# Kernel tuning notes

Measured on AMD Instinct MI355X. Metric: run time of the kernel, lower is better.

The kernel has to match this reference:

```python
import jax, jax.numpy as jnp
import numpy as np

NEG_SLOPE = 0.01  # torch F.leaky_relu default


def setup_inputs() -> dict:
    key = jax.random.key(0)
    k1, k2, k3, k4, k5 = jax.random.split(key, 5)
    N, E, IN_DIM, OUT_DIM = 100000, 1600000, 128, 64
    h = jax.random.normal(k1, (N, IN_DIM), dtype=jnp.float32)
    src = jax.random.randint(k2, (E,), 0, N, dtype=jnp.int64)
    dst = jax.random.randint(k3, (E,), 0, N, dtype=jnp.int64)
    # xavier_normal-ish scaled params
    W1 = jax.random.normal(k4, (OUT_DIM, IN_DIM), dtype=jnp.float32) * (2.0 / (IN_DIM + OUT_DIM)) ** 0.5
    Wa = jax.random.normal(k5, (1, 2 * OUT_DIM), dtype=jnp.float32) * (2.0 / (2 * OUT_DIM + 1)) ** 0.5
    return {"h": h, "src": src, "dst": dst, "W1": W1, "Wa": Wa}


def reference(h, src, dst, W1, Wa):
    N = h.shape[0]
    D = W1.shape[0]
    z = h @ W1.T  # [N, D]
    z_src = z[src]  # [E, D] gather
    z_dst = z[dst]  # [E, D] gather
    a_src, a_dst = Wa[0, :D], Wa[0, D:]
    # attn_fc(concat(z_src, z_dst)) == z_src@a_src + z_dst@a_dst
    e = z_src @ a_src + z_dst @ a_dst  # [E]
    e = jnp.where(e >= 0, e, NEG_SLOPE * e)  # leaky_relu
    # segment softmax over incoming edges of each dst node
    e_max = jax.ops.segment_max(e, dst, num_segments=N)
    e_max = jnp.where(jnp.isfinite(e_max), e_max, 0.0)  # empty segments
    e_exp = jnp.exp(e - e_max[dst])
    denom = jax.ops.segment_sum(e_exp, dst, num_segments=N)
    alpha = e_exp / jnp.maximum(denom, 1e-16)[dst]  # [E]
    # weighted scatter-sum of source messages
    h_out = jax.ops.segment_sum(alpha[:, None] * z_src, dst, num_segments=N)  # [N, D]
    return h_out
```

## Files before the change

kernel.cpp:

```cpp
#include <hip/hip_runtime.h>
#include <hip/hip_bf16.h>

#define NEG_SLOPE 0.01f
#define NPB 512
#define CHUNK 4096

typedef __attribute__((ext_vector_type(8))) short short8;
typedef __attribute__((ext_vector_type(4))) float f32x4;

__device__ __forceinline__ unsigned short f2bf_rne(float f) {
    unsigned u = __float_as_uint(f);
    u += 0x7FFFu + ((u >> 16) & 1u);
    return (unsigned short)(u >> 16);
}

__global__ __launch_bounds__(256, 4) void k_gp(
    const float* __restrict__ h, const float* __restrict__ W1,
    const float* __restrict__ Wa, unsigned short* __restrict__ zb,
    float* __restrict__ s, float* __restrict__ t, int N, int G1,
    const int* __restrict__ src, const int* __restrict__ dst,
    unsigned* __restrict__ gcur, unsigned* __restrict__ table,
    int E, int NBKT, int BCAP)
{
    __shared__ __align__(16) union SM {
        struct { short wsb[64 * 128]; short tbuf[4][16 * 64]; } g;
        struct {
            unsigned cnt[256]; unsigned exc[256]; unsigned sbuf[256];
            unsigned gbaseb[256]; unsigned stage[CHUNK];
            unsigned short bkt[CHUNK];
        } p;
    } sm;
    const int tid = threadIdx.x;

    if (blockIdx.x < (unsigned)G1) {
        const int nb = blockIdx.x * 256;
        const int w  = tid >> 6;
        const int l  = tid & 63;
        const int lr = l & 15;
        const int lc = l >> 4;
        const int rowbase = nb + w * 64;
        const float4* __restrict__ h4 = (const float4*)h;
        const float4* __restrict__ W14 = (const float4*)W1;

        float asrc[4], adst[4];
#pragma unroll
        for (int ni = 0; ni < 4; ++ni) {
            asrc[ni] = Wa[ni * 16 + lr];
            adst[ni] = Wa[64 + ni * 16 + lr];
        }

        float4 av[8];
        {
            const int myn = rowbase + lr;
#pragma unroll
            for (int ks = 0; ks < 4; ++ks) {
                const int kcb = ks * 4 + lc;
                if (myn < N) {
                    av[2 * ks]     = h4[(size_t)myn * 32 + kcb * 2];
                    av[2 * ks + 1] = h4[(size_t)myn * 32 + kcb * 2 + 1];
                } else {
                    av[2 * ks]     = make_float4(0.f, 0.f, 0.f, 0.f);
                    av[2 * ks + 1] = make_float4(0.f, 0.f, 0.f, 0.f);
                }
            }
        }

#pragma unroll
        for (int it = 0; it < 4; ++it) {
            const int q = tid + it * 256;
            const int r = q >> 4, cb = q & 15;
            float4 v0 = W14[(size_t)r * 32 + cb * 2];
            float4 v1 = W14[(size_t)r * 32 + cb * 2 + 1];
            short8 o;
            o[0]=f2bf_rne(v0.x); o[1]=f2bf_rne(v0.y); o[2]=f2bf_rne(v0.z); o[3]=f2bf_rne(v0.w);
            o[4]=f2bf_rne(v1.x); o[5]=f2bf_rne(v1.y); o[6]=f2bf_rne(v1.z); o[7]=f2bf_rne(v1.w);
            *(short8*)&sm.g.wsb[r * 128 + ((cb * 8) ^ ((r & 7) << 3))] = o;
        }
        __syncthreads();

        short* __restrict__ tb = sm.g.tbuf[w];

#pragma unroll
        for (int rg = 0; rg < 4; ++rg) {
            short8 afr[4];
#pragma unroll
            for (int ks = 0; ks < 4; ++ks) {
                const float4 v0 = av[2 * ks], v1 = av[2 * ks + 1];
                short8 o;
                o[0]=f2bf_rne(v0.x); o[1]=f2bf_rne(v0.y); o[2]=f2bf_rne(v0.z); o[3]=f2bf_rne(v0.w);
                o[4]=f2bf_rne(v1.x); o[5]=f2bf_rne(v1.y); o[6]=f2bf_rne(v1.z); o[7]=f2bf_rne(v1.w);
                afr[ks] = o;
            }
            if (rg < 3) {
                const int myn = rowbase + (rg + 1) * 16 + lr;
#pragma unroll
                for (int ks = 0; ks < 4; ++ks) {
                    const int kcb = ks * 4 + lc;
                    if (myn < N) {
                        av[2 * ks]     = h4[(size_t)myn * 32 + kcb * 2];
                        av[2 * ks + 1] = h4[(size_t)myn * 32 + kcb * 2 + 1];
                    } else {
                        av[2 * ks]     = make_float4(0.f, 0.f, 0.f, 0.f);
                        av[2 * ks + 1] = make_float4(0.f, 0.f, 0.f, 0.f);
                    }
                }
            }

            f32x4 acc[4];
#pragma unroll
            for (int ni = 0; ni < 4; ++ni) acc[ni] = (f32x4){0.f, 0.f, 0.f, 0.f};
#pragma unroll
            for (int ks = 0; ks < 4; ++ks) {
                const int kcb = ks * 4 + lc;
#pragma unroll
                for (int ni = 0; ni < 4; ++ni) {
                    const int wr = ni * 16 + lr;
                    const short8 bf = *(const short8*)&sm.g.wsb[wr * 128 + ((kcb * 8) ^ ((wr & 7) << 3))];
                    acc[ni] = __builtin_amdgcn_mfma_f32_16x16x32_bf16(afr[ks], bf, acc[ni], 0, 0, 0);
                }
            }

#pragma unroll
            for (int r = 0; r < 4; ++r) {
                float ps = 0.f, pt = 0.f;
#pragma unroll
                for (int ni = 0; ni < 4; ++ni) {
                    ps = fmaf(acc[ni][r], asrc[ni], ps);
                    pt = fmaf(acc[ni][r], adst[ni], pt);
                }
#pragma unroll
                for (int m = 1; m < 16; m <<= 1) {
                    ps += __shfl_xor(ps, m);
                    pt += __shfl_xor(pt, m);
                }
                const int node = rowbase + rg * 16 + lc * 4 + r;
                if (lr == 0 && node < N) { s[node] = ps; t[node] = pt; }
            }

#pragma unroll
            for (int ni = 0; ni < 4; ++ni) {
                const int col = ni * 16 + lr;
#pragma unroll
                for (int r = 0; r < 4; ++r) {
                    const int ro = lc * 4 + r;
                    tb[ro * 64 + (((col >> 3) ^ (ro & 7)) << 3) + (col & 7)]
                        = (short)f2bf_rne(acc[ni][r]);
                }
            }
            {
                const int ro = l >> 2;
                const int n = rowbase + rg * 16 + ro;
                if (n < N) {
#pragma unroll
                    for (int j = 0; j < 2; ++j) {
                        const int c = (l & 3) * 2 + j;
                        const short8 v = *(const short8*)&tb[ro * 64 + ((c ^ (ro & 7)) << 3)];
                        *(short8*)&zb[(size_t)n * 64 + c * 8] = v;
                    }
                }
            }
        }
    } else {
        const int e0 = (blockIdx.x - G1) * CHUNK;
        const int nE = min(CHUNK, E - e0);

        sm.p.cnt[tid] = 0u;
        __syncthreads();
        for (int i = tid; i < nE; i += 256)
            atomicAdd(&sm.p.cnt[(unsigned)dst[e0 + i] >> 9], 1u);
        __syncthreads();

        const unsigned myc = sm.p.cnt[tid];
        if (tid < NBKT && myc > 0u) sm.p.gbaseb[tid] = atomicAdd(&gcur[tid], myc);

        sm.p.sbuf[tid] = myc;
        __syncthreads();
        for (int off = 1; off < 256; off <<= 1) {
            unsigned x = (tid >= off) ? sm.p.sbuf[tid - off] : 0u;
            __syncthreads();
            sm.p.sbuf[tid] += x;
            __syncthreads();
        }
        sm.p.exc[tid] = sm.p.sbuf[tid] - myc;
        __syncthreads();
        sm.p.cnt[tid] = 0u;
        __syncthreads();

        for (int i = tid; i < nE; i += 256) {
            const unsigned d = (unsigned)dst[e0 + i];
            const unsigned b = d >> 9;
            const unsigned pos = sm.p.exc[b] + atomicAdd(&sm.p.cnt[b], 1u);
            sm.p.stage[pos] = ((unsigned)src[e0 + i] << 9) | (d & 511u);
            sm.p.bkt[pos] = (unsigned short)b;
        }
        __syncthreads();

        for (int i = tid; i < nE; i += 256) {
            const unsigned b = sm.p.bkt[i];
            const unsigned off = sm.p.gbaseb[b] + ((unsigned)i - sm.p.exc[b]);
            if (off < (unsigned)BCAP)
                table[(size_t)b * BCAP + off] = sm.p.stage[i];
        }
    }
}

__global__ __launch_bounds__(256) void k_sortb2(
    const unsigned* __restrict__ table, const unsigned* __restrict__ gcur,
    unsigned* __restrict__ edge_src,
    unsigned* __restrict__ offsets, unsigned* __restrict__ counts,
    int N, int NBKT, int BCAP)
{
    __shared__ unsigned ncnt[NPB];
    __shared__ unsigned nexc[NPB];
    __shared__ unsigned sbuf[NPB];
    __shared__ unsigned basesh;
    const int b = blockIdx.x;
    const int t = threadIdx.x;
    const int bc = min((int)gcur[b], BCAP);
    const size_t tb = (size_t)b * BCAP;

    {
        unsigned c = (t < NBKT) ? min(gcur[t], (unsigned)BCAP) : 0u;
        sbuf[t] = c;
        __syncthreads();
        for (int off = 1; off < 256; off <<= 1) {
            unsigned x = (t >= off) ? sbuf[t - off] : 0u;
            __syncthreads();
            sbuf[t] += x;
            __syncthreads();
        }
        if (t == 0) basesh = (b == 0) ? 0u : sbuf[b - 1];
        __syncthreads();
    }
    const unsigned base = basesh;
    __syncthreads();

    ncnt[t] = 0u; ncnt[t + 256] = 0u;
    __syncthreads();
    for (int i = t; i < bc; i += 256)
        atomicAdd(&ncnt[table[tb + i] & 511u], 1u);
    __syncthreads();

    const unsigned c0 = ncnt[t], c1 = ncnt[t + 256];
    sbuf[t] = c0; sbuf[t + 256] = c1;
    __syncthreads();
    for (int off = 1; off < NPB; off <<= 1) {
        unsigned x0 = (t >= off) ? sbuf[t - off] : 0u;
        unsigned x1 = (t + 256 >= off) ? sbuf[t + 256 - off] : 0u;
        __syncthreads();
        sbuf[t] += x0; sbuf[t + 256] += x1;
        __syncthreads();
    }
    nexc[t] = sbuf[t] - c0; nexc[t + 256] = sbuf[t + 256] - c1;
    __syncthreads();

    {
        const int n0 = b * NPB + t, n1 = n0 + 256;
        if (n0 < N) { offsets[n0] = base + nexc[t];        counts[n0] = c0; }
        if (n1 < N) { offsets[n1] = base + nexc[t + 256];  counts[n1] = c1; }
    }
    ncnt[t] = 0u; ncnt[t + 256] = 0u;
    __syncthreads();

    for (int i = t; i < bc; i += 256) {
        const unsigned v = table[tb + i];
        const unsigned l = v & 511u;
        const unsigned pos = nexc[l] + atomicAdd(&ncnt[l], 1u);
        edge_src[base + pos] = v >> 9;
    }
}

__global__ __launch_bounds__(256) void k_node(
    const unsigned* __restrict__ offsets, const unsigned* __restrict__ counts,
    const unsigned* __restrict__ edge_src,
    const float* __restrict__ s, const float* __restrict__ t,
    const unsigned short* __restrict__ zb, float* __restrict__ out, int N)
{
    const int tid = threadIdx.x;
    const int node = blockIdx.x * 16 + (tid >> 4);
    if (node >= N) return;
    const int wl    = tid & 63;
    const int gbase = wl & ~15;
    const int sub   = wl & 15;
    const int g2    = sub >> 3;
    const int l8    = sub & 7;

    const unsigned beg = offsets[node];
    const int cnt = (int)counts[node];
    if (cnt == 0) {
        if (sub < 8) {
            const float4 zz = make_float4(0.f, 0.f, 0.f, 0.f);
            *(float4*)&out[(size_t)node * 64 + sub * 8]     = zz;
            *(float4*)&out[(size_t)node * 64 + sub * 8 + 4] = zz;
        }
        return;
    }

    const float tn = t[node];
    const unsigned short* __restrict__ zrow = zb + l8 * 8;
    float dl = 0.f;
    float acc[8] = {0.f, 0.f, 0.f, 0.f, 0.f, 0.f, 0.f, 0.f};

    for (int base = 0; base < cnt; base += 16) {
        const int rem = min(16, cnt - base);
        int sj = 0;
        float p = 0.f;
        if (sub < rem) {
            sj = (int)edge_src[beg + base + sub];
            float e = s[sj] + tn;
            e = (e >= 0.f) ? e : NEG_SLOPE * e;
            p = __expf(e);
            dl += p;
        }
#pragma unroll
        for (int k = 0; k < 8; ++k) {
            const int j = g2 * 8 + k;
            const float pj  = __shfl(p, gbase + j);
            const int   sjj = __shfl(sj, gbase + j);
            const uint4 v = *(const uint4*)&zrow[(size_t)sjj * 64];
#define UNPK(u, d0) \
            acc[d0]     = fmaf(pj, __uint_as_float((u) << 16),          acc[d0]); \
            acc[d0 + 1] = fmaf(pj, __uint_as_float((u) & 0xFFFF0000u), acc[d0 + 1]);
            UNPK(v.x, 0) UNPK(v.y, 2) UNPK(v.z, 4) UNPK(v.w, 6)
#undef UNPK
        }
    }

#pragma unroll
    for (int c = 0; c < 8; ++c)
        acc[c] += __shfl_xor(acc[c], 8);
    float den = dl;
#pragma unroll
    for (int m = 1; m < 16; m <<= 1) den += __shfl_xor(den, m);

    if (sub < 8) {
        const float inv = 1.f / fmaxf(den, 1e-16f);
        float4 o0 = make_float4(acc[0] * inv, acc[1] * inv, acc[2] * inv, acc[3] * inv);
        float4 o1 = make_float4(acc[4] * inv, acc[5] * inv, acc[6] * inv, acc[7] * inv);
        *(float4*)&out[(size_t)node * 64 + sub * 8]     = o0;
        *(float4*)&out[(size_t)node * 64 + sub * 8 + 4] = o1;
    }
}

extern "C" void kernel_launch(void* const* d_in, const int* in_sizes, int n_in,
                              void* d_out, int out_size, void* d_ws, size_t ws_size,
                              hipStream_t stream) {
    const float* h   = (const float*)d_in[0];
    const int*   src = (const int*)d_in[1];
    const int*   dst = (const int*)d_in[2];
    const float* W1  = (const float*)d_in[3];
    const float* Wa  = (const float*)d_in[4];
    float* out = (float*)d_out;

    const int N = in_sizes[0] / 128;
    const int E = in_sizes[1];
    const int NBKT = (N + NPB - 1) / NPB;
    const int meanb = (E + NBKT - 1) / NBKT;
    int slack = 24 * (int)sqrtf((float)meanb) + 64;
    const int BCAP = meanb + slack;

    const int G1 = (N + 255) / 256;
    const int G2 = (E + CHUNK - 1) / CHUNK;

    unsigned short* zb = (unsigned short*)d_ws;
    float*    s        = (float*)(zb + (size_t)N * 64);
    float*    t        = s + N;
    unsigned* gcur     = (unsigned*)(t + N);
    unsigned* offsets  = gcur + NBKT;
    unsigned* counts   = offsets + N;
    unsigned* edge_src = counts + N;
    unsigned* table    = edge_src + E;

    hipMemsetAsync(gcur, 0, (size_t)NBKT * sizeof(unsigned), stream);

    k_gp<<<G1 + G2, 256, 0, stream>>>(h, W1, Wa, zb, s, t, N, G1,
                                      src, dst, gcur, table, E, NBKT, BCAP);
    k_sortb2<<<NBKT, 256, 0, stream>>>(table, gcur, edge_src, offsets, counts, N, NBKT, BCAP);
    k_node<<<(N + 15) / 16, 256, 0, stream>>>(offsets, counts, edge_src, s, t, zb, out, N);
}
```

Before: 99.15 us.

## Compute attention scores in node kernel from gathered bf16 z rows

```diff
diff --git a/kernel.cpp b/kernel.cpp
--- a/kernel.cpp
+++ b/kernel.cpp
@@ -16,8 +16,7 @@
 
 __global__ __launch_bounds__(256, 4) void k_gp(
     const float* __restrict__ h, const float* __restrict__ W1,
-    const float* __restrict__ Wa, unsigned short* __restrict__ zb,
-    float* __restrict__ s, float* __restrict__ t, int N, int G1,
+    unsigned short* __restrict__ zb, int N, int G1,
     const int* __restrict__ src, const int* __restrict__ dst,
     unsigned* __restrict__ gcur, unsigned* __restrict__ table,
     int E, int NBKT, int BCAP)
@@ -42,13 +41,6 @@
         const float4* __restrict__ h4 = (const float4*)h;
         const float4* __restrict__ W14 = (const float4*)W1;
 
-        float asrc[4], adst[4];
-#pragma unroll
-        for (int ni = 0; ni < 4; ++ni) {
-            asrc[ni] = Wa[ni * 16 + lr];
-            adst[ni] = Wa[64 + ni * 16 + lr];
-        }
-
         float4 av[8];
         {
             const int myn = rowbase + lr;
@@ -118,23 +110,6 @@
                     const short8 bf = *(const short8*)&sm.g.wsb[wr * 128 + ((kcb * 8) ^ ((wr & 7) << 3))];
                     acc[ni] = __builtin_amdgcn_mfma_f32_16x16x32_bf16(afr[ks], bf, acc[ni], 0, 0, 0);
                 }
-            }
-
-#pragma unroll
-            for (int r = 0; r < 4; ++r) {
-                float ps = 0.f, pt = 0.f;
-#pragma unroll
-                for (int ni = 0; ni < 4; ++ni) {
-                    ps = fmaf(acc[ni][r], asrc[ni], ps);
-                    pt = fmaf(acc[ni][r], adst[ni], pt);
-                }
-#pragma unroll
-                for (int m = 1; m < 16; m <<= 1) {
-                    ps += __shfl_xor(ps, m);
-                    pt += __shfl_xor(pt, m);
-                }
-                const int node = rowbase + rg * 16 + lc * 4 + r;
-                if (lr == 0 && node < N) { s[node] = ps; t[node] = pt; }
             }
 
 #pragma unroll
@@ -272,8 +247,7 @@
 
 __global__ __launch_bounds__(256) void k_node(
     const unsigned* __restrict__ offsets, const unsigned* __restrict__ counts,
-    const unsigned* __restrict__ edge_src,
-    const float* __restrict__ s, const float* __restrict__ t,
+    const unsigned* __restrict__ edge_src, const float* __restrict__ Wa,
     const unsigned short* __restrict__ zb, float* __restrict__ out, int N)
 {
     const int tid = threadIdx.x;
@@ -296,42 +270,70 @@
         return;
     }
 
-    const float tn = t[node];
-    const unsigned short* __restrict__ zrow = zb + l8 * 8;
+    const float4 as0 = *(const float4*)&Wa[l8 * 8];
+    const float4 as1 = *(const float4*)&Wa[l8 * 8 + 4];
+
+    float tn;
+    {
+        const uint2 zn = *(const uint2*)&zb[(size_t)node * 64 + sub * 4];
+        const float4 ad = *(const float4*)&Wa[64 + sub * 4];
+        float pd = __uint_as_float(zn.x << 16) * ad.x
+                 + __uint_as_float(zn.x & 0xFFFF0000u) * ad.y
+                 + __uint_as_float(zn.y << 16) * ad.z
+                 + __uint_as_float(zn.y & 0xFFFF0000u) * ad.w;
+#pragma unroll
+        for (int m = 1; m < 16; m <<= 1) pd += __shfl_xor(pd, m);
+        tn = pd;
+    }
+
     float dl = 0.f;
     float acc[8] = {0.f, 0.f, 0.f, 0.f, 0.f, 0.f, 0.f, 0.f};
 
     for (int base = 0; base < cnt; base += 16) {
-        const int rem = min(16, cnt - base);
+        const int rem = cnt - base;
         int sj = 0;
-        float p = 0.f;
-        if (sub < rem) {
-            sj = (int)edge_src[beg + base + sub];
-            float e = s[sj] + tn;
+        if (sub < rem) sj = (int)edge_src[beg + base + sub];
+
+        uint4 vv[8];
+#pragma unroll
+        for (int k = 0; k < 8; ++k) {
+            const int sjj = __shfl(sj, gbase + g2 * 8 + k);
+            vv[k] = *(const uint4*)&zb[(size_t)sjj * 64 + l8 * 8];
+        }
+#pragma unroll
+        for (int k = 0; k < 8; ++k) {
+            const uint4 v = vv[k];
+            const float z0 = __uint_as_float(v.x << 16);
+            const float z1 = __uint_as_float(v.x & 0xFFFF0000u);
+            const float z2 = __uint_as_float(v.y << 16);
+            const float z3 = __uint_as_float(v.y & 0xFFFF0000u);
+            const float z4 = __uint_as_float(v.z << 16);
+            const float z5 = __uint_as_float(v.z & 0xFFFF0000u);
+            const float z6 = __uint_as_float(v.w << 16);
+            const float z7 = __uint_as_float(v.w & 0xFFFF0000u);
+            float pd = z0 * as0.x;
+            pd = fmaf(z1, as0.y, pd); pd = fmaf(z2, as0.z, pd);
+            pd = fmaf(z3, as0.w, pd); pd = fmaf(z4, as1.x, pd);
+            pd = fmaf(z5, as1.y, pd); pd = fmaf(z6, as1.z, pd);
+            pd = fmaf(z7, as1.w, pd);
+            pd += __shfl_xor(pd, 1);
+            pd += __shfl_xor(pd, 2);
+            pd += __shfl_xor(pd, 4);
+            float e = pd + tn;
             e = (e >= 0.f) ? e : NEG_SLOPE * e;
-            p = __expf(e);
+            const float p = ((g2 << 3) + k < rem) ? __expf(e) : 0.f;
             dl += p;
-        }
-#pragma unroll
-        for (int k = 0; k < 8; ++k) {
-            const int j = g2 * 8 + k;
-            const float pj  = __shfl(p, gbase + j);
-            const int   sjj = __shfl(sj, gbase + j);
-            const uint4 v = *(const uint4*)&zrow[(size_t)sjj * 64];
-#define UNPK(u, d0) \
-            acc[d0]     = fmaf(pj, __uint_as_float((u) << 16),          acc[d0]); \
-            acc[d0 + 1] = fmaf(pj, __uint_as_float((u) & 0xFFFF0000u), acc[d0 + 1]);
-            UNPK(v.x, 0) UNPK(v.y, 2) UNPK(v.z, 4) UNPK(v.w, 6)
-#undef UNPK
+            acc[0] = fmaf(p, z0, acc[0]); acc[1] = fmaf(p, z1, acc[1]);
+            acc[2] = fmaf(p, z2, acc[2]); acc[3] = fmaf(p, z3, acc[3]);
+            acc[4] = fmaf(p, z4, acc[4]); acc[5] = fmaf(p, z5, acc[5]);
+            acc[6] = fmaf(p, z6, acc[6]); acc[7] = fmaf(p, z7, acc[7]);
         }
     }
 
 #pragma unroll
     for (int c = 0; c < 8; ++c)
         acc[c] += __shfl_xor(acc[c], 8);
-    float den = dl;
-#pragma unroll
-    for (int m = 1; m < 16; m <<= 1) den += __shfl_xor(den, m);
+    const float den = dl + __shfl_xor(dl, 8);
 
     if (sub < 8) {
         const float inv = 1.f / fmaxf(den, 1e-16f);
@@ -363,9 +365,7 @@
     const int G2 = (E + CHUNK - 1) / CHUNK;
 
     unsigned short* zb = (unsigned short*)d_ws;
-    float*    s        = (float*)(zb + (size_t)N * 64);
-    float*    t        = s + N;
-    unsigned* gcur     = (unsigned*)(t + N);
+    unsigned* gcur     = (unsigned*)(zb + (size_t)N * 64);
     unsigned* offsets  = gcur + NBKT;
     unsigned* counts   = offsets + N;
     unsigned* edge_src = counts + N;
@@ -373,8 +373,8 @@
 
     hipMemsetAsync(gcur, 0, (size_t)NBKT * sizeof(unsigned), stream);
 
-    k_gp<<<G1 + G2, 256, 0, stream>>>(h, W1, Wa, zb, s, t, N, G1,
+    k_gp<<<G1 + G2, 256, 0, stream>>>(h, W1, zb, N, G1,
                                       src, dst, gcur, table, E, NBKT, BCAP);
     k_sortb2<<<NBKT, 256, 0, stream>>>(table, gcur, edge_src, offsets, counts, N, NBKT, BCAP);
-    k_node<<<(N + 15) / 16, 256, 0, stream>>>(offsets, counts, edge_src, s, t, zb, out, N);
-}
+    k_node<<<(N + 15) / 16, 256, 0, stream>>>(offsets, counts, edge_src, Wa, zb, out, N);
+}
```

After: 103.4 us. 4.2% more time.

## Move attention score projection into sort kernel and batch gathers in node kernel

Applied to the files above, without the earlier changes.

```diff
diff --git a/kernel.cpp b/kernel.cpp
--- a/kernel.cpp
+++ b/kernel.cpp
@@ -16,8 +16,7 @@
 
 __global__ __launch_bounds__(256, 4) void k_gp(
     const float* __restrict__ h, const float* __restrict__ W1,
-    const float* __restrict__ Wa, unsigned short* __restrict__ zb,
-    float* __restrict__ s, float* __restrict__ t, int N, int G1,
+    unsigned short* __restrict__ zb, int N, int G1,
     const int* __restrict__ src, const int* __restrict__ dst,
     unsigned* __restrict__ gcur, unsigned* __restrict__ table,
     int E, int NBKT, int BCAP)
@@ -42,13 +41,6 @@
         const float4* __restrict__ h4 = (const float4*)h;
         const float4* __restrict__ W14 = (const float4*)W1;
 
-        float asrc[4], adst[4];
-#pragma unroll
-        for (int ni = 0; ni < 4; ++ni) {
-            asrc[ni] = Wa[ni * 16 + lr];
-            adst[ni] = Wa[64 + ni * 16 + lr];
-        }
-
         float4 av[8];
         {
             const int myn = rowbase + lr;
@@ -121,23 +113,6 @@
             }
 
 #pragma unroll
-            for (int r = 0; r < 4; ++r) {
-                float ps = 0.f, pt = 0.f;
-#pragma unroll
-                for (int ni = 0; ni < 4; ++ni) {
-                    ps = fmaf(acc[ni][r], asrc[ni], ps);
-                    pt = fmaf(acc[ni][r], adst[ni], pt);
-                }
-#pragma unroll
-                for (int m = 1; m < 16; m <<= 1) {
-                    ps += __shfl_xor(ps, m);
-                    pt += __shfl_xor(pt, m);
-                }
-                const int node = rowbase + rg * 16 + lc * 4 + r;
-                if (lr == 0 && node < N) { s[node] = ps; t[node] = pt; }
-            }
-
-#pragma unroll
             for (int ni = 0; ni < 4; ++ni) {
                 const int col = ni * 16 + lr;
 #pragma unroll
@@ -204,65 +179,103 @@
     }
 }
 
-__global__ __launch_bounds__(256) void k_sortb2(
+__global__ __launch_bounds__(256) void k_sp(
     const unsigned* __restrict__ table, const unsigned* __restrict__ gcur,
     unsigned* __restrict__ edge_src,
     unsigned* __restrict__ offsets, unsigned* __restrict__ counts,
+    const unsigned short* __restrict__ zb, const float* __restrict__ Wa,
+    float* __restrict__ s, float* __restrict__ t,
     int N, int NBKT, int BCAP)
 {
     __shared__ unsigned ncnt[NPB];
     __shared__ unsigned nexc[NPB];
     __shared__ unsigned sbuf[NPB];
     __shared__ unsigned basesh;
+    const int tid = threadIdx.x;
+
+    if (blockIdx.x >= (unsigned)NBKT) {
+        const int node = ((int)blockIdx.x - NBKT) * 32 + (tid >> 3);
+        const int l8 = tid & 7;
+        if (node < N) {
+            const uint4 v = *(const uint4*)&zb[(size_t)node * 64 + l8 * 8];
+            const float4 a0 = *(const float4*)&Wa[l8 * 8];
+            const float4 a1 = *(const float4*)&Wa[l8 * 8 + 4];
+            const float4 d0 = *(const float4*)&Wa[64 + l8 * 8];
+            const float4 d1 = *(const float4*)&Wa[64 + l8 * 8 + 4];
+            const float z0 = __uint_as_float(v.x << 16);
+            const float z1 = __uint_as_float(v.x & 0xFFFF0000u);
+            const float z2 = __uint_as_float(v.y << 16);
+            const float z3 = __uint_as_float(v.y & 0xFFFF0000u);
+            const float z4 = __uint_as_float(v.z << 16);
+            const float z5 = __uint_as_float(v.z & 0xFFFF0000u);
+            const float z6 = __uint_as_float(v.w << 16);
+            const float z7 = __uint_as_float(v.w & 0xFFFF0000u);
+            float ps = z0 * a0.x;
+            ps = fmaf(z1, a0.y, ps); ps = fmaf(z2, a0.z, ps); ps = fmaf(z3, a0.w, ps);
+            ps = fmaf(z4, a1.x, ps); ps = fmaf(z5, a1.y, ps); ps = fmaf(z6, a1.z, ps);
+            ps = fmaf(z7, a1.w, ps);
+            float pt = z0 * d0.x;
+            pt = fmaf(z1, d0.y, pt); pt = fmaf(z2, d0.z, pt); pt = fmaf(z3, d0.w, pt);
+            pt = fmaf(z4, d1.x, pt); pt = fmaf(z5, d1.y, pt); pt = fmaf(z6, d1.z, pt);
+            pt = fmaf(z7, d1.w, pt);
+#pragma unroll
+            for (int m = 1; m < 8; m <<= 1) {
+                ps += __shfl_xor(ps, m);
+                pt += __shfl_xor(pt, m);
+            }
+            if (l8 == 0) { s[node] = ps; t[node] = pt; }
+        }
+        return;
+    }
+
     const int b = blockIdx.x;
-    const int t = threadIdx.x;
     const int bc = min((int)gcur[b], BCAP);
     const size_t tb = (size_t)b * BCAP;
 
     {
-        unsigned c = (t < NBKT) ? min(gcur[t], (unsigned)BCAP) : 0u;
-        sbuf[t] = c;
+        unsigned c = (tid < NBKT) ? min(gcur[tid], (unsigned)BCAP) : 0u;
+        sbuf[tid] = c;
         __syncthreads();
         for (int off = 1; off < 256; off <<= 1) {
-            unsigned x = (t >= off) ? sbuf[t - off] : 0u;
+            unsigned x = (tid >= off) ? sbuf[tid - off] : 0u;
             __syncthreads();
-            sbuf[t] += x;
+            sbuf[tid] += x;
             __syncthreads();
         }
-        if (t == 0) basesh = (b == 0) ? 0u : sbuf[b - 1];
+        if (tid == 0) basesh = (b == 0) ? 0u : sbuf[b - 1];
         __syncthreads();
     }
     const unsigned base = basesh;
     __syncthreads();
 
-    ncnt[t] = 0u; ncnt[t + 256] = 0u;
-    __syncthreads();
-    for (int i = t; i < bc; i += 256)
+    ncnt[tid] = 0u; ncnt[tid + 256] = 0u;
+    __syncthreads();
+    for (int i = tid; i < bc; i += 256)
         atomicAdd(&ncnt[table[tb + i] & 511u], 1u);
     __syncthreads();
 
-    const unsigned c0 = ncnt[t], c1 = ncnt[t + 256];
-    sbuf[t] = c0; sbuf[t + 256] = c1;
+    const unsigned c0 = ncnt[tid], c1 = ncnt[tid + 256];
+    sbuf[tid] = c0; sbuf[tid + 256] = c1;
     __syncthreads();
     for (int off = 1; off < NPB; off <<= 1) {
-        unsigned x0 = (t >= off) ? sbuf[t - off] : 0u;
-        unsigned x1 = (t + 256 >= off) ? sbuf[t + 256 - off] : 0u;
-        __syncthreads();
-        sbuf[t] += x0; sbuf[t + 256] += x1;
-        __syncthreads();
-    }
-    nexc[t] = sbuf[t] - c0; nexc[t + 256] = sbuf[t + 256] - c1;
+        unsigned x0 = (tid >= off) ? sbuf[tid - off] : 0u;
+        unsigned x1 = (tid + 256 >= off) ? sbuf[tid + 256 - off] : 0u;
+        __syncthreads();
+        sbuf[tid] += x0; sbuf[tid + 256] += x1;
+        __syncthreads();
+    }
+    nexc[tid] = sbuf[tid] - c0; nexc[tid + 256] = sbuf[tid + 256] - c1;
     __syncthreads();
 
     {
-        const int n0 = b * NPB + t, n1 = n0 + 256;
-        if (n0 < N) { offsets[n0] = base + nexc[t];        counts[n0] = c0; }
-        if (n1 < N) { offsets[n1] = base + nexc[t + 256];  counts[n1] = c1; }
-    }
-    ncnt[t] = 0u; ncnt[t + 256] = 0u;
-    __syncthreads();
-
-    for (int i = t; i < bc; i += 256) {
+        const int n0 = b * NPB + tid, n1 = n0 + 256;
+        if (n0 < N) { offsets[n0] = base + nexc[tid];        counts[n0] = c0; }
+        if (n1 < N) { offsets[n1] = base + nexc[tid + 256];  counts[n1] = c1; }
+    }
+    ncnt[tid] = 0u; ncnt[tid + 256] = 0u;
+    __syncthreads();
+
+    for (int i = tid; i < bc; i += 256) {
         const unsigned v = table[tb + i];
         const unsigned l = v & 511u;
         const unsigned pos = nexc[l] + atomicAdd(&ncnt[l], 1u);
@@ -302,7 +315,7 @@
     float acc[8] = {0.f, 0.f, 0.f, 0.f, 0.f, 0.f, 0.f, 0.f};
 
     for (int base = 0; base < cnt; base += 16) {
-        const int rem = min(16, cnt - base);
+        const int rem = cnt - base;
         int sj = 0;
         float p = 0.f;
         if (sub < rem) {
@@ -312,12 +325,16 @@
             p = __expf(e);
             dl += p;
         }
+        uint4 vv[8];
 #pragma unroll
         for (int k = 0; k < 8; ++k) {
-            const int j = g2 * 8 + k;
-            const float pj  = __shfl(p, gbase + j);
-            const int   sjj = __shfl(sj, gbase + j);
-            const uint4 v = *(const uint4*)&zrow[(size_t)sjj * 64];
+            const int sjj = __shfl(sj, gbase + g2 * 8 + k);
+            vv[k] = *(const uint4*)&zrow[(size_t)sjj * 64];
+        }
+#pragma unroll
+        for (int k = 0; k < 8; ++k) {
+            const float pj = __shfl(p, gbase + g2 * 8 + k);
+            const uint4 v = vv[k];
 #define UNPK(u, d0) \
             acc[d0]     = fmaf(pj, __uint_as_float((u) << 16),          acc[d0]); \
             acc[d0 + 1] = fmaf(pj, __uint_as_float((u) & 0xFFFF0000u), acc[d0 + 1]);
@@ -361,6 +378,7 @@
 
     const int G1 = (N + 255) / 256;
     const int G2 = (E + CHUNK - 1) / CHUNK;
+    const int GST = (N + 31) / 32;
 
     unsigned short* zb = (unsigned short*)d_ws;
     float*    s        = (float*)(zb + (size_t)N * 64);
@@ -373,8 +391,9 @@
 
     hipMemsetAsync(gcur, 0, (size_t)NBKT * sizeof(unsigned), stream);
 
-    k_gp<<<G1 + G2, 256, 0, stream>>>(h, W1, Wa, zb, s, t, N, G1,
+    k_gp<<<G1 + G2, 256, 0, stream>>>(h, W1, zb, N, G1,
                                       src, dst, gcur, table, E, NBKT, BCAP);
-    k_sortb2<<<NBKT, 256, 0, stream>>>(table, gcur, edge_src, offsets, counts, N, NBKT, BCAP);
+    k_sp<<<NBKT + GST, 256, 0, stream>>>(table, gcur, edge_src, offsets, counts,
+                                         zb, Wa, s, t, N, NBKT, BCAP);
     k_node<<<(N + 15) / 16, 256, 0, stream>>>(offsets, counts, edge_src, s, t, zb, out, N);
 }
```

New measurement: 99.72 us. No clear change (+0.6%).

## Compute softmax numerators and denominators in sort kernel, batch gathers in node kernel

Applied to the files above, without the earlier changes.

```diff
diff --git a/kernel.cpp b/kernel.cpp
--- a/kernel.cpp
+++ b/kernel.cpp
@@ -204,76 +204,77 @@
     }
 }
 
-__global__ __launch_bounds__(256) void k_sortb2(
+__global__ __launch_bounds__(512) void k_sp(
     const unsigned* __restrict__ table, const unsigned* __restrict__ gcur,
-    unsigned* __restrict__ edge_src,
-    unsigned* __restrict__ offsets, unsigned* __restrict__ counts,
+    const float* __restrict__ s, const float* __restrict__ t,
+    uint2* __restrict__ edge_ps, unsigned* __restrict__ offsets,
+    unsigned* __restrict__ counts, float* __restrict__ invden,
     int N, int NBKT, int BCAP)
 {
-    __shared__ unsigned ncnt[NPB];
-    __shared__ unsigned nexc[NPB];
-    __shared__ unsigned sbuf[NPB];
+    __shared__ unsigned ncnt[NPB], nexc[NPB], scur[NPB], sbuf[NPB];
+    __shared__ float tlds[NPB], den[NPB];
     __shared__ unsigned basesh;
+    const int tid = threadIdx.x;
     const int b = blockIdx.x;
-    const int t = threadIdx.x;
     const int bc = min((int)gcur[b], BCAP);
-    const size_t tb = (size_t)b * BCAP;
+    const size_t tbo = (size_t)b * BCAP;
+    const int node = b * NPB + tid;
 
     {
-        unsigned c = (t < NBKT) ? min(gcur[t], (unsigned)BCAP) : 0u;
-        sbuf[t] = c;
-        __syncthreads();
-        for (int off = 1; off < 256; off <<= 1) {
-            unsigned x = (t >= off) ? sbuf[t - off] : 0u;
+        unsigned c = (tid < NBKT) ? min(gcur[tid], (unsigned)BCAP) : 0u;
+        sbuf[tid] = c;
+        __syncthreads();
+        for (int off = 1; off < NPB; off <<= 1) {
+            unsigned x = (tid >= off) ? sbuf[tid - off] : 0u;
             __syncthreads();
-            sbuf[t] += x;
+            sbuf[tid] += x;
             __syncthreads();
         }
-        if (t == 0) basesh = (b == 0) ? 0u : sbuf[b - 1];
-        __syncthreads();
-    }
+        if (tid == 0) basesh = (b == 0) ? 0u : sbuf[b - 1];
+    }
+    tlds[tid] = (node < N) ? t[node] : 0.f;
+    den[tid] = 0.f;
+    ncnt[tid] = 0u;
+    __syncthreads();
     const unsigned base = basesh;
-    __syncthreads();
-
-    ncnt[t] = 0u; ncnt[t + 256] = 0u;
-    __syncthreads();
-    for (int i = t; i < bc; i += 256)
-        atomicAdd(&ncnt[table[tb + i] & 511u], 1u);
-    __syncthreads();
-
-    const unsigned c0 = ncnt[t], c1 = ncnt[t + 256];
-    sbuf[t] = c0; sbuf[t + 256] = c1;
+
+    for (int i = tid; i < bc; i += NPB)
+        atomicAdd(&ncnt[table[tbo + i] & 511u], 1u);
+    __syncthreads();
+
+    const unsigned c0 = ncnt[tid];
+    sbuf[tid] = c0;
     __syncthreads();
     for (int off = 1; off < NPB; off <<= 1) {
-        unsigned x0 = (t >= off) ? sbuf[t - off] : 0u;
-        unsigned x1 = (t + 256 >= off) ? sbuf[t + 256 - off] : 0u;
-        __syncthreads();
-        sbuf[t] += x0; sbuf[t + 256] += x1;
-        __syncthreads();
-    }
-    nexc[t] = sbuf[t] - c0; nexc[t + 256] = sbuf[t + 256] - c1;
-    __syncthreads();
-
-    {
-        const int n0 = b * NPB + t, n1 = n0 + 256;
-        if (n0 < N) { offsets[n0] = base + nexc[t];        counts[n0] = c0; }
-        if (n1 < N) { offsets[n1] = base + nexc[t + 256];  counts[n1] = c1; }
-    }
-    ncnt[t] = 0u; ncnt[t + 256] = 0u;
-    __syncthreads();
-
-    for (int i = t; i < bc; i += 256) {
-        const unsigned v = table[tb + i];
+        unsigned x = (tid >= off) ? sbuf[tid - off] : 0u;
+        __syncthreads();
+        sbuf[tid] += x;
+        __syncthreads();
+    }
+    nexc[tid] = sbuf[tid] - c0;
+    scur[tid] = 0u;
+    __syncthreads();
+
+    if (node < N) { offsets[node] = base + nexc[tid]; counts[node] = c0; }
+
+    for (int i = tid; i < bc; i += NPB) {
+        const unsigned v = table[tbo + i];
         const unsigned l = v & 511u;
-        const unsigned pos = nexc[l] + atomicAdd(&ncnt[l], 1u);
-        edge_src[base + pos] = v >> 9;
-    }
+        const unsigned sj = v >> 9;
+        float e = s[sj] + tlds[l];
+        e = (e >= 0.f) ? e : NEG_SLOPE * e;
+        const float p = __expf(e);
+        const unsigned pos = nexc[l] + atomicAdd(&scur[l], 1u);
+        edge_ps[base + pos] = make_uint2(__float_as_uint(p), sj);
+        atomicAdd(&den[l], p);
+    }
+    __syncthreads();
+    if (node < N) invden[node] = 1.f / fmaxf(den[tid], 1e-16f);
 }
 
 __global__ __launch_bounds__(256) void k_node(
     const unsigned* __restrict__ offsets, const unsigned* __restrict__ counts,
-    const unsigned* __restrict__ edge_src,
-    const float* __restrict__ s, const float* __restrict__ t,
+    const uint2* __restrict__ edge_ps, const float* __restrict__ invden,
     const unsigned short* __restrict__ zb, float* __restrict__ out, int N)
 {
     const int tid = threadIdx.x;
@@ -296,28 +297,27 @@
         return;
     }
 
-    const float tn = t[node];
+    const float invd = invden[node];
     const unsigned short* __restrict__ zrow = zb + l8 * 8;
-    float dl = 0.f;
     float acc[8] = {0.f, 0.f, 0.f, 0.f, 0.f, 0.f, 0.f, 0.f};
 
     for (int base = 0; base < cnt; base += 16) {
-        const int rem = min(16, cnt - base);
-        int sj = 0;
-        float p = 0.f;
-        if (sub < rem) {
-            sj = (int)edge_src[beg + base + sub];
-            float e = s[sj] + tn;
-            e = (e >= 0.f) ? e : NEG_SLOPE * e;
-            p = __expf(e);
-            dl += p;
-        }
+        const int rem = cnt - base;
+        uint2 ep = make_uint2(0u, 0u);
+        if (sub < rem) ep = edge_ps[beg + base + sub];
+        const float p = __uint_as_float(ep.x);
+        const int  sj = (int)ep.y;
+
+        uint4 vv[8];
 #pragma unroll
         for (int k = 0; k < 8; ++k) {
-            const int j = g2 * 8 + k;
-            const float pj  = __shfl(p, gbase + j);
-            const int   sjj = __shfl(sj, gbase + j);
-            const uint4 v = *(const uint4*)&zrow[(size_t)sjj * 64];
+            const int sjj = __shfl(sj, gbase + g2 * 8 + k);
+            vv[k] = *(const uint4*)&zrow[(size_t)sjj * 64];
+        }
+#pragma unroll
+        for (int k = 0; k < 8; ++k) {
+            const float pj = __shfl(p, gbase + g2 * 8 + k);
+            const uint4 v = vv[k];
 #define UNPK(u, d0) \
             acc[d0]     = fmaf(pj, __uint_as_float((u) << 16),          acc[d0]); \
             acc[d0 + 1] = fmaf(pj, __uint_as_float((u) & 0xFFFF0000u), acc[d0 + 1]);
@@ -329,14 +329,10 @@
 #pragma unroll
     for (int c = 0; c < 8; ++c)
         acc[c] += __shfl_xor(acc[c], 8);
-    float den = dl;
-#pragma unroll
-    for (int m = 1; m < 16; m <<= 1) den += __shfl_xor(den, m);
 
     if (sub < 8) {
-        const float inv = 1.f / fmaxf(den, 1e-16f);
-        float4 o0 = make_float4(acc[0] * inv, acc[1] * inv, acc[2] * inv, acc[3] * inv);
-        float4 o1 = make_float4(acc[4] * inv, acc[5] * inv, acc[6] * inv, acc[7] * inv);
+        float4 o0 = make_float4(acc[0] * invd, acc[1] * invd, acc[2] * invd, acc[3] * invd);
+        float4 o1 = make_float4(acc[4] * invd, acc[5] * invd, acc[6] * invd, acc[7] * invd);
         *(float4*)&out[(size_t)node * 64 + sub * 8]     = o0;
         *(float4*)&out[(size_t)node * 64 + sub * 8 + 4] = o1;
     }
@@ -368,13 +364,15 @@
     unsigned* gcur     = (unsigned*)(t + N);
     unsigned* offsets  = gcur + NBKT;
     unsigned* counts   = offsets + N;
-    unsigned* edge_src = counts + N;
-    unsigned* table    = edge_src + E;
+    float*    invden   = (float*)(counts + N);
+    uint2*    edge_ps  = (uint2*)(invden + N);
+    unsigned* table    = (unsigned*)(edge_ps + E);
 
     hipMemsetAsync(gcur, 0, (size_t)NBKT * sizeof(unsigned), stream);
 
     k_gp<<<G1 + G2, 256, 0, stream>>>(h, W1, Wa, zb, s, t, N, G1,
                                       src, dst, gcur, table, E, NBKT, BCAP);
-    k_sortb2<<<NBKT, 256, 0, stream>>>(table, gcur, edge_src, offsets, counts, N, NBKT, BCAP);
-    k_node<<<(N + 15) / 16, 256, 0, stream>>>(offsets, counts, edge_src, s, t, zb, out, N);
-}
+    k_sp<<<NBKT, 512, 0, stream>>>(table, gcur, s, t, edge_ps, offsets, counts,
+                                   invden, N, NBKT, BCAP);
+    k_node<<<(N + 15) / 16, 256, 0, stream>>>(offsets, counts, edge_ps, invden, zb, out, N);
+}
```

Measured after the change: 95.19 us, median of 3. 4.0% less time.
